# Kernel optimization log

Hardware: AMD Instinct MI355X
Metric: run time of the kernel (lower is better)

The kernel has to match this reference:

```python
import jax, jax.numpy as jnp
import numpy as np


def setup_inputs() -> dict:
    key = jax.random.key(0)
    ks = jax.random.split(key, 10)
    B, C, W, H = 4, 128, 64, 64
    c_half = C // 2          # 64
    d_qk = c_half // 8       # 8 (ratio=8)
    c_out = c_half           # 64
    inp = {
        "x":   jax.random.normal(ks[0], (B, C, W, H), jnp.float32),
        # att2.query_conv (used for both q2 and k2)
        "wq2": jax.random.normal(ks[1], (d_qk, c_half), jnp.float32) * 0.05,
        "bq2": jax.random.normal(ks[2], (d_qk,), jnp.float32) * 0.05,
        # att3.query_conv (used for both q3 and k3)
        "wq3": jax.random.normal(ks[3], (d_qk, c_half), jnp.float32) * 0.05,
        "bq3": jax.random.normal(ks[4], (d_qk,), jnp.float32) * 0.05,
        # att3.value_conv
        "wv3": jax.random.normal(ks[5], (c_out, c_half), jnp.float32) * 0.05,
        "bv3": jax.random.normal(ks[6], (c_out,), jnp.float32) * 0.05,
        # gammas are zero-init in torch; use small random so output is non-trivial
        "gamma2": jax.random.normal(ks[7], (1,), jnp.float32) * 0.1,
        "gamma3": jax.random.normal(ks[8], (1,), jnp.float32) * 0.1,
    }
    return inp


def reference(x, wq2, bq2, wq3, bq3, wv3, bv3, gamma2, gamma3):
    B, C, W, H = x.shape
    c_half = C // 2
    N = W * H
    x3 = x[:, :c_half].reshape(B, c_half, N)   # [B, C/2, N]
    x2 = x[:, c_half:].reshape(B, c_half, N)

    def conv1x1(w, b, inp):  # [O,Ci] x [B,Ci,N] -> [B,O,N]
        return jnp.einsum('oc,bcn->bon', w, inp) + b[None, :, None]

    p2 = conv1x1(wq2, bq2, x2)   # [B, d, N]  (q2 and k2 share this projection)
    p3 = conv1x1(wq3, bq3, x3)   # [B, d, N]  (q3 and k3 share this projection)
    v3 = conv1x1(wv3, bv3, x3)   # [B, Cout, N]

    # energy: q3^T @ k  -> [B, N, N]; softmax over last dim (no scaling)
    att32 = jax.nn.softmax(jnp.einsum('bdm,bdn->bmn', p3, p2), axis=-1)
    att33 = jax.nn.softmax(jnp.einsum('bdm,bdn->bmn', p3, p3), axis=-1)

    # out = v3 @ att^T : out[b,c,m] = sum_n v3[b,c,n] * att[b,m,n]
    out32 = jnp.einsum('bcn,bmn->bcm', v3, att32)
    out33 = jnp.einsum('bcn,bmn->bcm', v3, att33)

    out = gamma2 * out32 + gamma3 * out33 + x3   # add=True
    return out.reshape(B, c_half, W, H)
```

## Files before the change

kernel.cpp:

```cpp
#include <hip/hip_runtime.h>

#define NN 4096
#define BB 4

typedef short v8s __attribute__((ext_vector_type(8)));
typedef float v4f __attribute__((ext_vector_type(4)));

__device__ __forceinline__ float bf2f(unsigned short u) {
  union { unsigned int i; float f; } v;
  v.i = ((unsigned int)u) << 16;
  return v.f;
}
__device__ __forceinline__ unsigned short f2bf(float f) {
  union { float f; unsigned int i; } v;
  v.f = f;
  unsigned int r = v.i + 0x7FFFu + ((v.i >> 16) & 1u);
  return (unsigned short)(r >> 16);
}
__device__ __forceinline__ unsigned int pkbf(float hi, float lo) {
  union { float f; unsigned int u; } a, b;
  a.f = hi; b.f = lo;
  return __builtin_amdgcn_perm(a.u, b.u, 0x07060302u);
}

__device__ __forceinline__ float ldv(const float* p, size_t i) { return p[i]; }
__device__ __forceinline__ float ldv(const unsigned short* p, size_t i) { return bf2f(p[i]); }

template <int NPL>
__device__ __forceinline__ bool sniff_f32(const unsigned short* xu) {
  const int lane = threadIdx.x & 63;
  int cnt = 0;
  #pragma unroll
  for (int j = 0; j < NPL; j++) {
    unsigned short u = xu[lane * NPL + j];
    cnt += (((u >> 7) & 0xFF) >= 137) ? 1 : 0;
  }
  #pragma unroll
  for (int s = 1; s < 64; s <<= 1) cnt += __shfl_xor(cnt, s);
  return cnt > NPL;
}

#define QK_SCALE 1.2011224087864498f

template <typename T>
__device__ __forceinline__ void proj_body(
    const T* __restrict__ x,
    const T* __restrict__ wq2, const T* __restrict__ bq2,
    const T* __restrict__ wq3, const T* __restrict__ bq3,
    const T* __restrict__ wv3, const T* __restrict__ bv3,
    unsigned short* __restrict__ p2bf, unsigned short* __restrict__ p3bf,
    unsigned short* __restrict__ v3bf)
{
  const int tid  = threadIdx.x;
  const int lane = tid & 63;
  const int w    = tid >> 6;
  const int q    = lane >> 4;
  const int l15  = lane & 15;
  const int bid  = blockIdx.x;
  const int b    = bid >> 6;
  const int nt   = bid & 63;
  const int n    = (nt << 6) + w * 16 + l15;

  v8s aq2[2], aq3[2], av[4][2];
  #pragma unroll
  for (int ks = 0; ks < 2; ks++) {
    const int c0 = ks * 32 + q * 8;
    #pragma unroll
    for (int j = 0; j < 8; j++) {
      const int wrow = (l15 < 8) ? l15 : 0;
      const float w2 = ldv(wq2, wrow * 64 + c0 + j);
      const float w3 = ldv(wq3, wrow * 64 + c0 + j);
      aq2[ks][j] = (l15 < 8) ? (short)f2bf(QK_SCALE * w2) : (short)0;
      aq3[ks][j] = (l15 < 8) ? (short)f2bf(QK_SCALE * w3) : (short)0;
    }
    #pragma unroll
    for (int t = 0; t < 4; t++) {
      #pragma unroll
      for (int j = 0; j < 8; j++)
        av[t][ks][j] = (short)f2bf(ldv(wv3, (t * 16 + l15) * 64 + c0 + j));
    }
  }

  v4f ap2, ap3, avc[4];
  #pragma unroll
  for (int r = 0; r < 4; r++) {
    const int ob = (q < 2) ? q * 4 + r : 0;
    const float b2 = ldv(bq2, ob), b3 = ldv(bq3, ob);
    ap2[r] = (q < 2) ? QK_SCALE * b2 : 0.f;
    ap3[r] = (q < 2) ? QK_SCALE * b3 : 0.f;
  }
  #pragma unroll
  for (int t = 0; t < 4; t++)
    #pragma unroll
    for (int r = 0; r < 4; r++) avc[t][r] = ldv(bv3, t * 16 + q * 4 + r);

  const size_t xb = (size_t)b * 128 * NN + n;
  #pragma unroll
  for (int ks = 0; ks < 2; ks++) {
    const int c0 = ks * 32 + q * 8;
    v8s bx2, bx3;
    #pragma unroll
    for (int j = 0; j < 8; j++) {
      bx2[j] = (short)f2bf(ldv(x, xb + (size_t)(64 + c0 + j) * NN));
      bx3[j] = (short)f2bf(ldv(x, xb + (size_t)(c0 + j) * NN));
    }
    ap2 = __builtin_amdgcn_mfma_f32_16x16x32_bf16(aq2[ks], bx2, ap2, 0, 0, 0);
    ap3 = __builtin_amdgcn_mfma_f32_16x16x32_bf16(aq3[ks], bx3, ap3, 0, 0, 0);
    #pragma unroll
    for (int t = 0; t < 4; t++)
      avc[t] = __builtin_amdgcn_mfma_f32_16x16x32_bf16(av[t][ks], bx3, avc[t], 0, 0, 0);
  }

  if (q < 2) {
    uint2 u2, u3;
    u2.x = pkbf(ap2[1], ap2[0]); u2.y = pkbf(ap2[3], ap2[2]);
    u3.x = pkbf(ap3[1], ap3[0]); u3.y = pkbf(ap3[3], ap3[2]);
    *(uint2*)(p2bf + ((size_t)b * NN + n) * 8 + q * 4) = u2;
    *(uint2*)(p3bf + ((size_t)b * NN + n) * 8 + q * 4) = u3;
  }
  #pragma unroll
  for (int t = 0; t < 4; t++)
    #pragma unroll
    for (int r = 0; r < 4; r++)
      v3bf[((size_t)b * 64 + t * 16 + q * 4 + r) * NN + n] = f2bf(avc[t][r]);
}

__global__ __launch_bounds__(256) void proj_kernel(
    const void* __restrict__ x,
    const void* __restrict__ wq2, const void* __restrict__ bq2,
    const void* __restrict__ wq3, const void* __restrict__ bq3,
    const void* __restrict__ wv3, const void* __restrict__ bv3,
    unsigned short* __restrict__ p2bf, unsigned short* __restrict__ p3bf,
    unsigned short* __restrict__ v3bf)
{
  const bool f32 = sniff_f32<16>((const unsigned short*)x);
  if (f32)
    proj_body<float>((const float*)x, (const float*)wq2, (const float*)bq2,
                     (const float*)wq3, (const float*)bq3,
                     (const float*)wv3, (const float*)bv3, p2bf, p3bf, v3bf);
  else
    proj_body<unsigned short>((const unsigned short*)x, (const unsigned short*)wq2,
                              (const unsigned short*)bq2, (const unsigned short*)wq3,
                              (const unsigned short*)bq3, (const unsigned short*)wv3,
                              (const unsigned short*)bv3, p2bf, p3bf, v3bf);
}

__global__ __launch_bounds__(256, 4) void attn_kernel(
    const unsigned short* __restrict__ p2bf, const unsigned short* __restrict__ p3bf,
    const unsigned short* __restrict__ v3bf,
    unsigned short* __restrict__ wso, float* __restrict__ wsl,
    int log2S, int nChunks)
{
  __shared__ unsigned short vtile[64 * 72];
  __shared__ unsigned short p2t[64 * 8];
  __shared__ unsigned short p3t[64 * 8];
  __shared__ unsigned short etile[4][2][16 * 72];

  const int tid  = threadIdx.x;
  const int lane = tid & 63;
  const int w    = tid >> 6;
  const int q    = lane >> 4;
  const int l15  = lane & 15;
  const int bid  = blockIdx.x;
  const int S    = 1 << log2S;
  const int seg  = bid & (S - 1);
  const int t    = bid >> log2S;
  const int mt   = t & 63;
  const int b    = t >> 6;
  const int m    = (mt << 6) + w * 16 + l15;

  v8s b3m = {0, 0, 0, 0, 0, 0, 0, 0};
  if (q == 0) b3m = *(const v8s*)(p3bf + ((size_t)b * NN + m) * 8);

  const v8s ones = {16256, 16256, 16256, 16256, 16256, 16256, 16256, 16256};

  v4f acc32[4], acc33[4], lac2, lac3;
  #pragma unroll
  for (int ct = 0; ct < 4; ct++)
    #pragma unroll
    for (int r = 0; r < 4; r++) { acc32[ct][r] = 0.f; acc33[ct][r] = 0.f; }
  #pragma unroll
  for (int r = 0; r < 4; r++) { lac2[r] = 0.f; lac3[r] = 0.f; }

  const int n_base = seg * (nChunks * 64);
  unsigned short* et2 = &etile[w][0][0];
  unsigned short* et3 = &etile[w][1][0];

  const int vrow = tid >> 3, vseg = tid & 7;
  uint4 vreg0, vreg1, preg;

  {
    const int n0 = n_base;
    vreg0 = *(const uint4*)(v3bf + ((size_t)b * 64 + vrow) * NN + n0 + vseg * 8);
    vreg1 = *(const uint4*)(v3bf + ((size_t)b * 64 + (vrow + 32)) * NN + n0 + vseg * 8);
    if (tid < 64)       preg = *(const uint4*)(p2bf + ((size_t)b * NN + n0 + tid) * 8);
    else if (tid < 128) preg = *(const uint4*)(p3bf + ((size_t)b * NN + n0 + (tid - 64)) * 8);
  }

  for (int ci = 0; ci < nChunks; ci++) {
    __syncthreads();
    *(uint4*)(vtile + vrow * 72 + vseg * 8)        = vreg0;
    *(uint4*)(vtile + (vrow + 32) * 72 + vseg * 8) = vreg1;
    if (tid < 64)       *(uint4*)(p2t + tid * 8)        = preg;
    else if (tid < 128) *(uint4*)(p3t + (tid - 64) * 8) = preg;
    __syncthreads();

    if (ci + 1 < nChunks) {
      const int n1 = n_base + (ci + 1) * 64;
      vreg0 = *(const uint4*)(v3bf + ((size_t)b * 64 + vrow) * NN + n1 + vseg * 8);
      vreg1 = *(const uint4*)(v3bf + ((size_t)b * 64 + (vrow + 32)) * NN + n1 + vseg * 8);
      if (tid < 64)       preg = *(const uint4*)(p2bf + ((size_t)b * NN + n1 + tid) * 8);
      else if (tid < 128) preg = *(const uint4*)(p3bf + ((size_t)b * NN + n1 + (tid - 64)) * 8);
    }

    #pragma unroll
    for (int s = 0; s < 4; s++) {
      v8s A2 = {0, 0, 0, 0, 0, 0, 0, 0};
      v8s A3 = {0, 0, 0, 0, 0, 0, 0, 0};
      if (q == 0) {
        A2 = *(const v8s*)(p2t + (s * 16 + l15) * 8);
        A3 = *(const v8s*)(p3t + (s * 16 + l15) * 8);
      }
      v4f z = {0.f, 0.f, 0.f, 0.f};
      v4f e2 = __builtin_amdgcn_mfma_f32_16x16x32_bf16(A2, b3m, z, 0, 0, 0);
      v4f e3 = __builtin_amdgcn_mfma_f32_16x16x32_bf16(A3, b3m, z, 0, 0, 0);
      float t2[4], t3[4];
      #pragma unroll
      for (int r = 0; r < 4; r++) {
        t2[r] = exp2f(e2[r]);
        t3[r] = exp2f(e3[r]);
      }
      uint2 w2, w3;
      w2.x = pkbf(t2[1], t2[0]); w2.y = pkbf(t2[3], t2[2]);
      w3.x = pkbf(t3[1], t3[0]); w3.y = pkbf(t3[3], t3[2]);
      *(uint2*)(et2 + l15 * 72 + s * 16 + q * 4) = w2;
      *(uint2*)(et3 + l15 * 72 + s * 16 + q * 4) = w3;
    }

    #pragma unroll
    for (int kh = 0; kh < 2; kh++) {
      v8s at2 = *(const v8s*)(et2 + l15 * 72 + kh * 32 + q * 8);
      v8s at3 = *(const v8s*)(et3 + l15 * 72 + kh * 32 + q * 8);
      lac2 = __builtin_amdgcn_mfma_f32_16x16x32_bf16(ones, at2, lac2, 0, 0, 0);
      lac3 = __builtin_amdgcn_mfma_f32_16x16x32_bf16(ones, at3, lac3, 0, 0, 0);
      #pragma unroll
      for (int ct = 0; ct < 4; ct++) {
        v8s va = *(const v8s*)(vtile + (ct * 16 + l15) * 72 + kh * 32 + q * 8);
        acc32[ct] = __builtin_amdgcn_mfma_f32_16x16x32_bf16(va, at2, acc32[ct], 0, 0, 0);
        acc33[ct] = __builtin_amdgcn_mfma_f32_16x16x32_bf16(va, at3, acc33[ct], 0, 0, 0);
      }
    }
  }

  if (q == 0) {
    wsl[((size_t)bid * 2 + 0) * 64 + w * 16 + l15] = lac2[0];
    wsl[((size_t)bid * 2 + 1) * 64 + w * 16 + l15] = lac3[0];
  }
  const int m6 = w * 16 + l15;
  #pragma unroll
  for (int ct = 0; ct < 4; ct++) {
    uint2 o2, o3;
    o2.x = pkbf(acc32[ct][1], acc32[ct][0]); o2.y = pkbf(acc32[ct][3], acc32[ct][2]);
    o3.x = pkbf(acc33[ct][1], acc33[ct][0]); o3.y = pkbf(acc33[ct][3], acc33[ct][2]);
    *(uint2*)(wso + (((size_t)bid * 2 + 0) * 64 + m6) * 64 + ct * 16 + q * 4) = o2;
    *(uint2*)(wso + (((size_t)bid * 2 + 1) * 64 + m6) * 64 + ct * 16 + q * 4) = o3;
  }
}

__global__ __launch_bounds__(256) void reduce_kernel(
    const unsigned short* __restrict__ wso, const float* __restrict__ wsl,
    const void* __restrict__ x, const void* __restrict__ g2p,
    const void* __restrict__ g3p, void* __restrict__ out, int S)
{
  __shared__ float t32[64 * 65];
  __shared__ float t33[64 * 65];
  __shared__ float iL2s[64], iL3s[64];

  const bool f32 = sniff_f32<4>((const unsigned short*)x);
  const int tid = threadIdx.x;
  const int mt  = blockIdx.x & 63;
  const int b   = blockIdx.x >> 6;
  const size_t blk0 = (size_t)((b << 6) + mt) * S;

  #pragma unroll
  for (int k = 0; k < 4; k++) {
    const int idx = tid + k * 256;
    const int m6 = idx >> 4;
    const int cg = idx & 15;
    float o2[4] = {0.f, 0.f, 0.f, 0.f}, o3[4] = {0.f, 0.f, 0.f, 0.f};
    for (int sg = 0; sg < S; sg++) {
      const uint2 u2 = *(const uint2*)(wso + ((blk0 + sg) * 2 + 0) * 4096 + m6 * 64 + cg * 4);
      const uint2 u3 = *(const uint2*)(wso + ((blk0 + sg) * 2 + 1) * 4096 + m6 * 64 + cg * 4);
      union { unsigned int u; float f; } c0, c1, c2, c3;
      c0.u = u2.x << 16; c1.u = u2.x & 0xFFFF0000u; c2.u = u2.y << 16; c3.u = u2.y & 0xFFFF0000u;
      o2[0] += c0.f; o2[1] += c1.f; o2[2] += c2.f; o2[3] += c3.f;
      c0.u = u3.x << 16; c1.u = u3.x & 0xFFFF0000u; c2.u = u3.y << 16; c3.u = u3.y & 0xFFFF0000u;
      o3[0] += c0.f; o3[1] += c1.f; o3[2] += c2.f; o3[3] += c3.f;
    }
    #pragma unroll
    for (int j = 0; j < 4; j++) {
      t32[m6 * 65 + cg * 4 + j] = o2[j];
      t33[m6 * 65 + cg * 4 + j] = o3[j];
    }
  }
  if (tid < 64) {
    float L2 = 0.f, L3 = 0.f;
    for (int sg = 0; sg < S; sg++) {
      L2 += wsl[((blk0 + sg) * 2 + 0) * 64 + tid];
      L3 += wsl[((blk0 + sg) * 2 + 1) * 64 + tid];
    }
    const float g2 = f32 ? ((const float*)g2p)[0] : bf2f(((const unsigned short*)g2p)[0]);
    const float g3 = f32 ? ((const float*)g3p)[0] : bf2f(((const unsigned short*)g3p)[0]);
    iL2s[tid] = g2 / L2;
    iL3s[tid] = g3 / L3;
  }
  __syncthreads();

  const int m6 = tid & 63;
  const int ch = tid >> 6;
  #pragma unroll
  for (int k = 0; k < 16; k++) {
    const int c = k * 4 + ch;
    const size_t xi = ((size_t)b * 128 + c) * NN + (mt << 6) + m6;
    const float xv = f32 ? ((const float*)x)[xi] : bf2f(((const unsigned short*)x)[xi]);
    const float val = fmaf(iL2s[m6], t32[m6 * 65 + c], fmaf(iL3s[m6], t33[m6 * 65 + c], xv));
    const size_t oi = ((size_t)b * 64 + c) * NN + (mt << 6) + m6;
    if (f32) ((float*)out)[oi] = val;
    else     ((unsigned short*)out)[oi] = f2bf(val);
  }
}

extern "C" void kernel_launch(void* const* d_in, const int* in_sizes, int n_in,
                              void* d_out, int out_size, void* d_ws, size_t ws_size,
                              hipStream_t stream) {
  const void* x   = d_in[0];
  const void* wq2 = d_in[1];
  const void* bq2 = d_in[2];
  const void* wq3 = d_in[3];
  const void* bq3 = d_in[4];
  const void* wv3 = d_in[5];
  const void* bv3 = d_in[6];
  const void* g2  = d_in[7];
  const void* g3  = d_in[8];

  unsigned short* p2bf = (unsigned short*)d_ws;
  unsigned short* p3bf = p2bf + (size_t)BB * NN * 8;
  unsigned short* v3bf = p3bf + (size_t)BB * NN * 8;
  const size_t base = 2 * (size_t)BB * NN * 8 * 2 + (size_t)BB * 64 * NN * 2;

  const size_t per_blk = 512 + 16384;
  int S = 1, log2S = 0;
  if      (ws_size >= base + (size_t)256 * 8 * per_blk) { S = 8; log2S = 3; }
  else if (ws_size >= base + (size_t)256 * 4 * per_blk) { S = 4; log2S = 2; }
  else if (ws_size >= base + (size_t)256 * 2 * per_blk) { S = 2; log2S = 1; }

  float* wsl = (float*)((char*)d_ws + base);
  unsigned short* wso = (unsigned short*)((char*)wsl + (size_t)256 * S * 512);
  const int nChunks = 64 / S;

  proj_kernel<<<dim3(BB * 64), dim3(256), 0, stream>>>(
      x, wq2, bq2, wq3, bq3, wv3, bv3, p2bf, p3bf, v3bf);
  attn_kernel<<<dim3(BB * 64 * S), dim3(256), 0, stream>>>(
      p2bf, p3bf, v3bf, wso, wsl, log2S, nChunks);
  reduce_kernel<<<dim3(BB * 64), dim3(256), 0, stream>>>(
      wso, wsl, x, g2, g3, d_out, S);
}
```

Baseline: 148.8 us.

## Stage projection inputs through LDS, use fast exp2, split reduce across more blocks

The projection kernel now loads x, the value weights and the query weights cooperatively into padded shared-memory tiles, converting them to bf16 once, and then reads MFMA operands from LDS. This replaces strided per-lane global loads and repeated weight conversion. The attention kernel swaps exp2f for the hardware exp2 builtin, which drops the accuracy wrapper. The reduce kernel launches four times as many blocks, each handling 16 rows, to raise parallelism. Shared-memory use in the projection kernel goes up and an extra barrier is added.

```diff
diff --git a/kernel.cpp b/kernel.cpp
--- a/kernel.cpp
+++ b/kernel.cpp
@@ -51,6 +51,12 @@
     unsigned short* __restrict__ p2bf, unsigned short* __restrict__ p3bf,
     unsigned short* __restrict__ v3bf)
 {
+  __shared__ unsigned short xt3[64 * 72];
+  __shared__ unsigned short xt2[64 * 72];
+  __shared__ unsigned short wvs[64 * 72];
+  __shared__ unsigned short wq2s[8 * 72];
+  __shared__ unsigned short wq3s[8 * 72];
+
   const int tid  = threadIdx.x;
   const int lane = tid & 63;
   const int w    = tid >> 6;
@@ -59,26 +65,42 @@
   const int bid  = blockIdx.x;
   const int b    = bid >> 6;
   const int nt   = bid & 63;
-  const int n    = (nt << 6) + w * 16 + l15;
-
+
+  #pragma unroll
+  for (int i = 0; i < 16; i++) {
+    const int idx = tid + i * 256;
+    wvs[(idx >> 6) * 72 + (idx & 63)] = f2bf(ldv(wv3, idx));
+  }
+  #pragma unroll
+  for (int i = 0; i < 4; i++) {
+    const int idx = tid + i * 256;
+    if (idx < 512) {
+      wq2s[(idx >> 6) * 72 + (idx & 63)] = f2bf(QK_SCALE * ldv(wq2, idx));
+    } else {
+      const int t2 = idx - 512;
+      wq3s[(t2 >> 6) * 72 + (t2 & 63)] = f2bf(QK_SCALE * ldv(wq3, t2));
+    }
+  }
+  const size_t xB = (size_t)b * 128 * NN + ((size_t)nt << 6);
+  #pragma unroll
+  for (int i = 0; i < 16; i++) {
+    const int idx = tid + i * 256;
+    const int c = idx >> 6, n = idx & 63;
+    xt3[n * 72 + c] = f2bf(ldv(x, xB + (size_t)c * NN + n));
+    xt2[n * 72 + c] = f2bf(ldv(x, xB + (size_t)(64 + c) * NN + n));
+  }
+  __syncthreads();
+
+  const v8s vz = {0, 0, 0, 0, 0, 0, 0, 0};
   v8s aq2[2], aq3[2], av[4][2];
   #pragma unroll
   for (int ks = 0; ks < 2; ks++) {
-    const int c0 = ks * 32 + q * 8;
-    #pragma unroll
-    for (int j = 0; j < 8; j++) {
-      const int wrow = (l15 < 8) ? l15 : 0;
-      const float w2 = ldv(wq2, wrow * 64 + c0 + j);
-      const float w3 = ldv(wq3, wrow * 64 + c0 + j);
-      aq2[ks][j] = (l15 < 8) ? (short)f2bf(QK_SCALE * w2) : (short)0;
-      aq3[ks][j] = (l15 < 8) ? (short)f2bf(QK_SCALE * w3) : (short)0;
-    }
-    #pragma unroll
-    for (int t = 0; t < 4; t++) {
-      #pragma unroll
-      for (int j = 0; j < 8; j++)
-        av[t][ks][j] = (short)f2bf(ldv(wv3, (t * 16 + l15) * 64 + c0 + j));
-    }
+    const int co = ks * 32 + q * 8;
+    aq2[ks] = (l15 < 8) ? *(const v8s*)(wq2s + l15 * 72 + co) : vz;
+    aq3[ks] = (l15 < 8) ? *(const v8s*)(wq3s + l15 * 72 + co) : vz;
+    #pragma unroll
+    for (int t = 0; t < 4; t++)
+      av[t][ks] = *(const v8s*)(wvs + (t * 16 + l15) * 72 + co);
   }
 
   v4f ap2, ap3, avc[4];
@@ -94,16 +116,12 @@
     #pragma unroll
     for (int r = 0; r < 4; r++) avc[t][r] = ldv(bv3, t * 16 + q * 4 + r);
 
-  const size_t xb = (size_t)b * 128 * NN + n;
+  const int nloc = w * 16 + l15;
   #pragma unroll
   for (int ks = 0; ks < 2; ks++) {
-    const int c0 = ks * 32 + q * 8;
-    v8s bx2, bx3;
-    #pragma unroll
-    for (int j = 0; j < 8; j++) {
-      bx2[j] = (short)f2bf(ldv(x, xb + (size_t)(64 + c0 + j) * NN));
-      bx3[j] = (short)f2bf(ldv(x, xb + (size_t)(c0 + j) * NN));
-    }
+    const int co = ks * 32 + q * 8;
+    v8s bx2 = *(const v8s*)(xt2 + nloc * 72 + co);
+    v8s bx3 = *(const v8s*)(xt3 + nloc * 72 + co);
     ap2 = __builtin_amdgcn_mfma_f32_16x16x32_bf16(aq2[ks], bx2, ap2, 0, 0, 0);
     ap3 = __builtin_amdgcn_mfma_f32_16x16x32_bf16(aq3[ks], bx3, ap3, 0, 0, 0);
     #pragma unroll
@@ -111,6 +129,7 @@
       avc[t] = __builtin_amdgcn_mfma_f32_16x16x32_bf16(av[t][ks], bx3, avc[t], 0, 0, 0);
   }
 
+  const int n = (nt << 6) + nloc;
   if (q < 2) {
     uint2 u2, u3;
     u2.x = pkbf(ap2[1], ap2[0]); u2.y = pkbf(ap2[3], ap2[2]);
@@ -227,8 +246,8 @@
       float t2[4], t3[4];
       #pragma unroll
       for (int r = 0; r < 4; r++) {
-        t2[r] = exp2f(e2[r]);
-        t3[r] = exp2f(e3[r]);
+        t2[r] = __builtin_amdgcn_exp2f(e2[r]);
+        t3[r] = __builtin_amdgcn_exp2f(e3[r]);
       }
       uint2 w2, w3;
       w2.x = pkbf(t2[1], t2[0]); w2.y = pkbf(t2[3], t2[2]);
@@ -272,21 +291,22 @@
     const void* __restrict__ x, const void* __restrict__ g2p,
     const void* __restrict__ g3p, void* __restrict__ out, int S)
 {
-  __shared__ float t32[64 * 65];
-  __shared__ float t33[64 * 65];
-  __shared__ float iL2s[64], iL3s[64];
+  __shared__ float t32[16 * 65];
+  __shared__ float t33[16 * 65];
+  __shared__ float iL2s[16], iL3s[16];
 
   const bool f32 = sniff_f32<4>((const unsigned short*)x);
   const int tid = threadIdx.x;
-  const int mt  = blockIdx.x & 63;
-  const int b   = blockIdx.x >> 6;
+  const int bid = blockIdx.x;
+  const int mq  = bid & 3;
+  const int mt  = (bid >> 2) & 63;
+  const int b   = bid >> 8;
   const size_t blk0 = (size_t)((b << 6) + mt) * S;
 
-  #pragma unroll
-  for (int k = 0; k < 4; k++) {
-    const int idx = tid + k * 256;
-    const int m6 = idx >> 4;
-    const int cg = idx & 15;
+  const int lr = tid >> 4;
+  const int m6 = mq * 16 + lr;
+  const int cg = tid & 15;
+  {
     float o2[4] = {0.f, 0.f, 0.f, 0.f}, o3[4] = {0.f, 0.f, 0.f, 0.f};
     for (int sg = 0; sg < S; sg++) {
       const uint2 u2 = *(const uint2*)(wso + ((blk0 + sg) * 2 + 0) * 4096 + m6 * 64 + cg * 4);
@@ -299,15 +319,16 @@
     }
     #pragma unroll
     for (int j = 0; j < 4; j++) {
-      t32[m6 * 65 + cg * 4 + j] = o2[j];
-      t33[m6 * 65 + cg * 4 + j] = o3[j];
-    }
-  }
-  if (tid < 64) {
+      t32[lr * 65 + cg * 4 + j] = o2[j];
+      t33[lr * 65 + cg * 4 + j] = o3[j];
+    }
+  }
+  if (tid < 16) {
+    const int mm = mq * 16 + tid;
     float L2 = 0.f, L3 = 0.f;
     for (int sg = 0; sg < S; sg++) {
-      L2 += wsl[((blk0 + sg) * 2 + 0) * 64 + tid];
-      L3 += wsl[((blk0 + sg) * 2 + 1) * 64 + tid];
+      L2 += wsl[((blk0 + sg) * 2 + 0) * 64 + mm];
+      L3 += wsl[((blk0 + sg) * 2 + 1) * 64 + mm];
     }
     const float g2 = f32 ? ((const float*)g2p)[0] : bf2f(((const unsigned short*)g2p)[0]);
     const float g3 = f32 ? ((const float*)g3p)[0] : bf2f(((const unsigned short*)g3p)[0]);
@@ -316,15 +337,16 @@
   }
   __syncthreads();
 
-  const int m6 = tid & 63;
-  const int ch = tid >> 6;
-  #pragma unroll
-  for (int k = 0; k < 16; k++) {
-    const int c = k * 4 + ch;
-    const size_t xi = ((size_t)b * 128 + c) * NN + (mt << 6) + m6;
+  const int ml = tid & 15;
+  const int cb = tid >> 4;
+  const int mg = (mt << 6) + mq * 16 + ml;
+  #pragma unroll
+  for (int j = 0; j < 4; j++) {
+    const int c = cb * 4 + j;
+    const size_t xi = ((size_t)b * 128 + c) * NN + mg;
     const float xv = f32 ? ((const float*)x)[xi] : bf2f(((const unsigned short*)x)[xi]);
-    const float val = fmaf(iL2s[m6], t32[m6 * 65 + c], fmaf(iL3s[m6], t33[m6 * 65 + c], xv));
-    const size_t oi = ((size_t)b * 64 + c) * NN + (mt << 6) + m6;
+    const float val = fmaf(iL2s[ml], t32[ml * 65 + c], fmaf(iL3s[ml], t33[ml * 65 + c], xv));
+    const size_t oi = ((size_t)b * 64 + c) * NN + mg;
     if (f32) ((float*)out)[oi] = val;
     else     ((unsigned short*)out)[oi] = f2bf(val);
   }
@@ -362,6 +384,6 @@
       x, wq2, bq2, wq3, bq3, wv3, bv3, p2bf, p3bf, v3bf);
   attn_kernel<<<dim3(BB * 64 * S), dim3(256), 0, stream>>>(
       p2bf, p3bf, v3bf, wso, wsl, log2S, nChunks);
-  reduce_kernel<<<dim3(BB * 64), dim3(256), 0, stream>>>(
+  reduce_kernel<<<dim3(BB * 64 * 4), dim3(256), 0, stream>>>(
       wso, wsl, x, g2, g3, d_out, S);
 }
```

After: 126.6 us (median of 2 runs). 14.9% less time.
